# Kernel optimization log

Hardware: AMD Instinct MI355X
Metric: run time of the kernel (lower is better)

The kernel has to match this reference:

```python
import math
import jax, jax.numpy as jnp
import numpy as np

D_MODEL = 1024
HEADS = 16
B, S = 4, 2048


def setup_inputs() -> dict:
    key = jax.random.key(0)
    ks = jax.random.split(key, 8)
    scale = 1.0 / math.sqrt(D_MODEL)
    return {
        "q": jax.random.normal(ks[0], (B, S, D_MODEL), dtype=jnp.float32),
        "k": jax.random.normal(ks[1], (B, S, D_MODEL), dtype=jnp.float32),
        "v": jax.random.normal(ks[2], (B, S, D_MODEL), dtype=jnp.float32),
        "mask": jax.random.randint(ks[3], (B, S), 0, 2).astype(jnp.bool_),
        "alibi_mask": jax.random.normal(ks[4], (1, HEADS, S, S), dtype=jnp.float32),
        "Wq": jax.random.normal(ks[5], (D_MODEL, D_MODEL), dtype=jnp.float32) * scale,
        "Wk": jax.random.normal(ks[6], (D_MODEL, D_MODEL), dtype=jnp.float32) * scale,
        "Wv": jax.random.normal(ks[7], (D_MODEL, D_MODEL), dtype=jnp.float32) * scale,
    }


def _split_heads(x):
    b, s, d = x.shape
    return x.reshape(b, s, HEADS, d // HEADS).transpose(0, 2, 1, 3)  # [B,H,S,hd]


def reference(q, k, v, mask, alibi_mask, Wq, Wk, Wv):
    # QKV projections (Linear, no bias)
    qh = _split_heads(q @ Wq)
    kh = _split_heads(k @ Wk)
    vh = _split_heads(v @ Wv)
    depth = qh.shape[-1]
    # naive full attention matrix [B,H,Sq,Sk]
    w = jnp.einsum("bhqd,bhkd->bhqk", qh, kh) / math.sqrt(depth)
    # mask: [B,Sk] -> [B,1,1,Sk], True = masked
    w = jnp.where(mask[:, None, None, :], -jnp.inf, w)
    w = w + alibi_mask
    a = jax.nn.softmax(w, axis=-1)  # dropout p=0 -> identity
    out = jnp.einsum("bhqk,bhkd->bhqd", a, vh)
    # combine heads -> [B,S,D]
    out = out.transpose(0, 2, 1, 3).reshape(q.shape[0], q.shape[1], -1)
    return (out, a)
```

## Files before the change

kernel.cpp:

```cpp
#include <hip/hip_runtime.h>
#include <hip/hip_bf16.h>
#include <math.h>

constexpr int B  = 4;
constexpr int S  = 2048;
constexpr int D  = 1024;
constexpr int H  = 16;
constexpr int HD = 64;
constexpr float LOG2E  = 1.4426950408889634f;
constexpr float SCALE2 = 0.125f * LOG2E;

using f32x4 = __attribute__((ext_vector_type(4))) float;
using s16x8 = __attribute__((ext_vector_type(8))) short;
using u16x8 = __attribute__((ext_vector_type(8))) unsigned short;
using u16x4 = __attribute__((ext_vector_type(4))) unsigned short;

__device__ __forceinline__ unsigned short f2bf(float f) {
    union { float f; unsigned u; } x; x.f = f;
    unsigned r = x.u + 0x7fffu + ((x.u >> 16) & 1u);
    return (unsigned short)(r >> 16);
}
__device__ __forceinline__ unsigned short f2bf_fast(float f) {
    union { float f; unsigned u; } x; x.f = f;
    return (unsigned short)((x.u + 0x8000u) >> 16);
}
__device__ __forceinline__ float bf2f(unsigned short h) {
    union { unsigned u; float f; } x; x.u = ((unsigned)h) << 16;
    return x.f;
}
__device__ __forceinline__ float fexp2(float x) {
#if __has_builtin(__builtin_amdgcn_exp2f)
    return __builtin_amdgcn_exp2f(x);
#else
    return __expf(x * 0.6931471805599453f);
#endif
}

#define MFMA_BF16(Af, Bf, Cf) __builtin_amdgcn_mfma_f32_16x16x32_bf16(Af, Bf, Cf, 0, 0, 0)

__global__ __launch_bounds__(256) void k_wt(const float* __restrict__ W,
                                            unsigned short* __restrict__ Wt) {
    __shared__ unsigned short T[64][68];
    const int k0 = blockIdx.x * 64, n0 = blockIdx.y * 64;
    const int t = threadIdx.x;
    {
        const int kr = t >> 4, nc4 = (t & 15) * 4;
        for (int rr = 0; rr < 4; ++rr) {
            const int kk = kr + rr * 16;
            f32x4 wv = *reinterpret_cast<const f32x4*>(&W[(size_t)(k0 + kk) * D + n0 + nc4]);
#pragma unroll
            for (int j = 0; j < 4; ++j) T[nc4 + j][kk] = f2bf(wv[j]);
        }
    }
    __syncthreads();
    {
        const int nr = t >> 4, kc4 = (t & 15) * 4;
        for (int rr = 0; rr < 4; ++rr) {
            const int nn = nr + rr * 16;
            u16x4 o;
#pragma unroll
            for (int j = 0; j < 4; ++j) o[j] = T[nn][kc4 + j];
            *reinterpret_cast<u16x4*>(&Wt[(size_t)(n0 + nn) * D + k0 + kc4]) = o;
        }
    }
}

__global__ __launch_bounds__(256) void k_proj_mfma(const float* __restrict__ X,
                                                   const unsigned short* __restrict__ Wt,
                                                   unsigned short* __restrict__ Y) {
    __shared__ alignas(16) unsigned short As[128][72];
    __shared__ alignas(16) unsigned short Bs[128][72];
    const int bm = blockIdx.y * 128, bn = blockIdx.x * 128;
    const int t = threadIdx.x, w = t >> 6, l = t & 63;
    const int wr = w >> 1, wc = w & 1;
    const int lr = l & 15, lg = l >> 4;
    f32x4 acc[4][4] = {};

    for (int k0 = 0; k0 < D; k0 += 64) {
        {
            const int c4 = (t & 15) * 4;
            int row = t >> 4;
            for (int rr = 0; rr < 8; ++rr, row += 16) {
                f32x4 xv = *reinterpret_cast<const f32x4*>(&X[(size_t)(bm + row) * D + k0 + c4]);
                u16x4 hv;
#pragma unroll
                for (int j = 0; j < 4; ++j) hv[j] = f2bf(xv[j]);
                *reinterpret_cast<u16x4*>(&As[row][c4]) = hv;
            }
        }
        for (int i = 0; i < 4; ++i) {
            const int idx = t + i * 256;
            const int row = idx >> 3, c8 = (idx & 7) * 8;
            *reinterpret_cast<u16x8*>(&Bs[row][c8]) =
                *reinterpret_cast<const u16x8*>(&Wt[(size_t)(bn + row) * D + k0 + c8]);
        }
        __syncthreads();
#pragma unroll
        for (int kk = 0; kk < 2; ++kk) {
            s16x8 af[4], bf[4];
#pragma unroll
            for (int f = 0; f < 4; ++f) {
                af[f] = *reinterpret_cast<const s16x8*>(&As[wr * 64 + f * 16 + lr][kk * 32 + lg * 8]);
                bf[f] = *reinterpret_cast<const s16x8*>(&Bs[wc * 64 + f * 16 + lr][kk * 32 + lg * 8]);
            }
#pragma unroll
            for (int fm = 0; fm < 4; ++fm)
#pragma unroll
                for (int fn = 0; fn < 4; ++fn)
                    acc[fm][fn] = MFMA_BF16(af[fm], bf[fn], acc[fm][fn]);
        }
        __syncthreads();
    }
#pragma unroll
    for (int fm = 0; fm < 4; ++fm)
#pragma unroll
        for (int fn = 0; fn < 4; ++fn)
#pragma unroll
            for (int r = 0; r < 4; ++r) {
                const int m = bm + wr * 64 + fm * 16 + lg * 4 + r;
                const int n = bn + wc * 64 + fn * 16 + lr;
                const int b = m >> 11, s = m & (S - 1);
                const int h = n >> 6, e = n & 63;
                Y[(((size_t)(b * H + h) * S) + s) * HD + e] = f2bf(acc[fm][fn][r]);
            }
}

__global__ __launch_bounds__(256) void k_projv_mfma(const float* __restrict__ X,
                                                    const unsigned short* __restrict__ Wt,
                                                    unsigned short* __restrict__ VT) {
    __shared__ alignas(16) unsigned short SM[2][128][72];
    unsigned short (*As)[72] = SM[0];
    unsigned short (*Bs)[72] = SM[1];
    const int bm = blockIdx.y * 128, bn = blockIdx.x * 128;
    const int t = threadIdx.x, w = t >> 6, l = t & 63;
    const int wr = w >> 1, wc = w & 1;
    const int lr = l & 15, lg = l >> 4;
    f32x4 acc[4][4] = {};

    for (int k0 = 0; k0 < D; k0 += 64) {
        {
            const int c4 = (t & 15) * 4;
            int row = t >> 4;
            for (int rr = 0; rr < 8; ++rr, row += 16) {
                f32x4 xv = *reinterpret_cast<const f32x4*>(&X[(size_t)(bm + row) * D + k0 + c4]);
                u16x4 hv;
#pragma unroll
                for (int j = 0; j < 4; ++j) hv[j] = f2bf(xv[j]);
                *reinterpret_cast<u16x4*>(&As[row][c4]) = hv;
            }
        }
        for (int i = 0; i < 4; ++i) {
            const int idx = t + i * 256;
            const int row = idx >> 3, c8 = (idx & 7) * 8;
            *reinterpret_cast<u16x8*>(&Bs[row][c8]) =
                *reinterpret_cast<const u16x8*>(&Wt[(size_t)(bn + row) * D + k0 + c8]);
        }
        __syncthreads();
#pragma unroll
        for (int kk = 0; kk < 2; ++kk) {
            s16x8 af[4], bf[4];
#pragma unroll
            for (int f = 0; f < 4; ++f) {
                af[f] = *reinterpret_cast<const s16x8*>(&As[wr * 64 + f * 16 + lr][kk * 32 + lg * 8]);
                bf[f] = *reinterpret_cast<const s16x8*>(&Bs[wc * 64 + f * 16 + lr][kk * 32 + lg * 8]);
            }
#pragma unroll
            for (int fm = 0; fm < 4; ++fm)
#pragma unroll
                for (int fn = 0; fn < 4; ++fn)
                    acc[fm][fn] = MFMA_BF16(af[fm], bf[fn], acc[fm][fn]);
        }
        __syncthreads();
    }
    unsigned short (*T)[144] = reinterpret_cast<unsigned short(*)[144]>(&SM[0][0][0]);
#pragma unroll
    for (int fm = 0; fm < 4; ++fm)
#pragma unroll
        for (int fn = 0; fn < 4; ++fn)
#pragma unroll
            for (int r = 0; r < 4; ++r)
                T[wc * 64 + fn * 16 + lr][wr * 64 + fm * 16 + lg * 4 + r] = f2bf(acc[fm][fn][r]);
    __syncthreads();
    const int b = bm >> 11, s0 = bm & (S - 1);
    for (int it = 0; it < 8; ++it) {
        const int idx = t + it * 256;
        const int row = idx >> 4, c8 = (idx & 15) * 8;
        const int h = (bn + row) >> 6, e = (bn + row) & 63;
        *reinterpret_cast<u16x8*>(&VT[((size_t)(b * H + h) * HD + e) * S + s0 + c8]) =
            *reinterpret_cast<const u16x8*>(&T[row][c8]);
    }
}

__global__ __launch_bounds__(256) void k_abf16(const float* __restrict__ A,
                                               unsigned short* __restrict__ O) {
    const size_t N = (size_t)H * S * S;
    const size_t stride = (size_t)gridDim.x * 256 * 8;
    for (size_t i = ((size_t)blockIdx.x * 256 + threadIdx.x) * 8; i < N; i += stride) {
        f32x4 a0 = *reinterpret_cast<const f32x4*>(&A[i]);
        f32x4 a1 = *reinterpret_cast<const f32x4*>(&A[i + 4]);
        u16x8 o;
#pragma unroll
        for (int j = 0; j < 4; ++j) {
            o[j]     = f2bf(a0[j] * LOG2E);
            o[4 + j] = f2bf(a1[j] * LOG2E);
        }
        *reinterpret_cast<u16x8*>(&O[i]) = o;
    }
}

template <bool ABF16>
__global__ __launch_bounds__(512, 4) void k_sumexp(
    const unsigned short* __restrict__ QH, const unsigned short* __restrict__ KH,
    const float* __restrict__ ALIBI, const unsigned short* __restrict__ ABF,
    const int* __restrict__ MASK, float* __restrict__ INVL) {
    __shared__ alignas(16) unsigned short Ks[64][72];
    __shared__ alignas(16) unsigned short ALs[128][72];

    const int bh = blockIdx.y, b = bh >> 4, h = bh & 15;
    const int q0 = blockIdx.x * 128;
    const int t = threadIdx.x, w = t >> 6, ln = t & 63;
    const int lr = ln & 15, lg = ln >> 4;
    const unsigned short NEGBIG = f2bf(-1e30f);
    const size_t hoff = (size_t)h * S * S;

    const unsigned short* Kb = KH + (size_t)bh * S * HD;

    s16x8 qf[2];
#pragma unroll
    for (int kk = 0; kk < 2; ++kk)
        qf[kk] = *reinterpret_cast<const s16x8*>(
            &QH[((size_t)bh * S + q0 + w * 16 + lr) * HD + kk * 32 + lg * 8]);

    float psum = 0.f;

    for (int k0 = 0; k0 < S; k0 += 64) {
        {
            const int row = t >> 3, c8 = (t & 7) * 8;
            *reinterpret_cast<u16x8*>(&Ks[row][c8]) =
                *reinterpret_cast<const u16x8*>(&Kb[(size_t)(k0 + row) * HD + c8]);
        }
#pragma unroll
        for (int i = 0; i < 2; ++i) {
            const int idx = t + i * 512, row = idx >> 3, c8 = (idx & 7) * 8;
            int4 m0 = *reinterpret_cast<const int4*>(&MASK[b * S + k0 + c8]);
            int4 m1 = *reinterpret_cast<const int4*>(&MASK[b * S + k0 + c8 + 4]);
            u16x8 av;
            if constexpr (ABF16) {
                av = *reinterpret_cast<const u16x8*>(&ABF[hoff + (size_t)(q0 + row) * S + k0 + c8]);
            } else {
                f32x4 a0 = *reinterpret_cast<const f32x4*>(&ALIBI[hoff + (size_t)(q0 + row) * S + k0 + c8]);
                f32x4 a1 = *reinterpret_cast<const f32x4*>(&ALIBI[hoff + (size_t)(q0 + row) * S + k0 + c8 + 4]);
#pragma unroll
                for (int j = 0; j < 4; ++j) {
                    av[j] = f2bf(a0[j] * LOG2E);
                    av[4 + j] = f2bf(a1[j] * LOG2E);
                }
            }
            u16x8 sv;
            sv[0] = m0.x ? NEGBIG : av[0];
            sv[1] = m0.y ? NEGBIG : av[1];
            sv[2] = m0.z ? NEGBIG : av[2];
            sv[3] = m0.w ? NEGBIG : av[3];
            sv[4] = m1.x ? NEGBIG : av[4];
            sv[5] = m1.y ? NEGBIG : av[5];
            sv[6] = m1.z ? NEGBIG : av[6];
            sv[7] = m1.w ? NEGBIG : av[7];
            *reinterpret_cast<u16x8*>(&ALs[row][c8]) = sv;
        }
        __syncthreads();

        f32x4 acc[4] = {};
#pragma unroll
        for (int kk = 0; kk < 2; ++kk)
#pragma unroll
            for (int fn = 0; fn < 4; ++fn) {
                s16x8 kf = *reinterpret_cast<const s16x8*>(&Ks[fn * 16 + lr][kk * 32 + lg * 8]);
                acc[fn] = MFMA_BF16(kf, qf[kk], acc[fn]);
            }
#pragma unroll
        for (int fn = 0; fn < 4; ++fn) {
            u16x4 alv = *reinterpret_cast<const u16x4*>(&ALs[w * 16 + lr][fn * 16 + lg * 4]);
            f32x4 al;
#pragma unroll
            for (int j = 0; j < 4; ++j) al[j] = bf2f(alv[j]);
            f32x4 sv = acc[fn] * SCALE2 + al;
            psum += fexp2(sv[0]) + fexp2(sv[1]) + fexp2(sv[2]) + fexp2(sv[3]);
        }
        __syncthreads();
    }

    psum += __shfl_xor(psum, 16, 64);
    psum += __shfl_xor(psum, 32, 64);
    if (lg == 0)
        INVL[(size_t)bh * S + q0 + w * 16 + lr] = 1.0f / psum;
}

template <bool ABF16>
__global__ __launch_bounds__(512, 4) void k_attn(
    const unsigned short* __restrict__ QH, const unsigned short* __restrict__ KH,
    const unsigned short* __restrict__ VT, const float* __restrict__ ALIBI,
    const unsigned short* __restrict__ ABF, const int* __restrict__ MASK,
    const float* __restrict__ INVL, float* __restrict__ Aout,
    float* __restrict__ OUT) {
    __shared__ alignas(16) unsigned short Ks[64][72];
    __shared__ alignas(16) unsigned short Vs[64][72];
    __shared__ alignas(16) unsigned short ALs[128][72];
    __shared__ alignas(16) unsigned short Ps[128][72];

    const int bh = blockIdx.y, b = bh >> 4, h = bh & 15;
    const int q0 = blockIdx.x * 128;
    const int t = threadIdx.x, w = t >> 6, ln = t & 63;
    const int lr = ln & 15, lg = ln >> 4;
    const unsigned short NEGBIG = f2bf(-1e30f);
    const size_t hoff = (size_t)h * S * S;

    const unsigned short* Kb = KH + (size_t)bh * S * HD;
    const unsigned short* Vb = VT + (size_t)bh * HD * S;

    s16x8 qf[2];
#pragma unroll
    for (int kk = 0; kk < 2; ++kk)
        qf[kk] = *reinterpret_cast<const s16x8*>(
            &QH[((size_t)bh * S + q0 + w * 16 + lr) * HD + kk * 32 + lg * 8]);

    const float invl = INVL[(size_t)bh * S + q0 + w * 16 + lr];
    float* arow = Aout + ((size_t)bh * S + q0 + w * 16 + lr) * S;

    f32x4 oacc[4] = {};

    for (int k0 = 0; k0 < S; k0 += 64) {
        {
            const int row = t >> 3, c8 = (t & 7) * 8;
            *reinterpret_cast<u16x8*>(&Ks[row][c8]) =
                *reinterpret_cast<const u16x8*>(&Kb[(size_t)(k0 + row) * HD + c8]);
            *reinterpret_cast<u16x8*>(&Vs[row][c8]) =
                *reinterpret_cast<const u16x8*>(&Vb[(size_t)row * S + k0 + c8]);
        }
#pragma unroll
        for (int i = 0; i < 2; ++i) {
            const int idx = t + i * 512, row = idx >> 3, c8 = (idx & 7) * 8;
            int4 m0 = *reinterpret_cast<const int4*>(&MASK[b * S + k0 + c8]);
            int4 m1 = *reinterpret_cast<const int4*>(&MASK[b * S + k0 + c8 + 4]);
            u16x8 av;
            if constexpr (ABF16) {
                av = *reinterpret_cast<const u16x8*>(&ABF[hoff + (size_t)(q0 + row) * S + k0 + c8]);
            } else {
                f32x4 a0 = *reinterpret_cast<const f32x4*>(&ALIBI[hoff + (size_t)(q0 + row) * S + k0 + c8]);
                f32x4 a1 = *reinterpret_cast<const f32x4*>(&ALIBI[hoff + (size_t)(q0 + row) * S + k0 + c8 + 4]);
#pragma unroll
                for (int j = 0; j < 4; ++j) {
                    av[j] = f2bf(a0[j] * LOG2E);
                    av[4 + j] = f2bf(a1[j] * LOG2E);
                }
            }
            u16x8 sv;
            sv[0] = m0.x ? NEGBIG : av[0];
            sv[1] = m0.y ? NEGBIG : av[1];
            sv[2] = m0.z ? NEGBIG : av[2];
            sv[3] = m0.w ? NEGBIG : av[3];
            sv[4] = m1.x ? NEGBIG : av[4];
            sv[5] = m1.y ? NEGBIG : av[5];
            sv[6] = m1.z ? NEGBIG : av[6];
            sv[7] = m1.w ? NEGBIG : av[7];
            *reinterpret_cast<u16x8*>(&ALs[row][c8]) = sv;
        }
        __syncthreads();

        f32x4 acc[4] = {};
#pragma unroll
        for (int kk = 0; kk < 2; ++kk)
#pragma unroll
            for (int fn = 0; fn < 4; ++fn) {
                s16x8 kf = *reinterpret_cast<const s16x8*>(&Ks[fn * 16 + lr][kk * 32 + lg * 8]);
                acc[fn] = MFMA_BF16(kf, qf[kk], acc[fn]);
            }

#pragma unroll
        for (int fn = 0; fn < 4; ++fn) {
            u16x4 alv = *reinterpret_cast<const u16x4*>(&ALs[w * 16 + lr][fn * 16 + lg * 4]);
            f32x4 al;
#pragma unroll
            for (int j = 0; j < 4; ++j) al[j] = bf2f(alv[j]);
            f32x4 sv = acc[fn] * SCALE2 + al;
            f32x4 p;
#pragma unroll
            for (int j = 0; j < 4; ++j) p[j] = fexp2(sv[j]);
            p *= invl;
            __builtin_nontemporal_store(
                p, reinterpret_cast<f32x4*>(arow + k0 + fn * 16 + lg * 4));
            u16x4 pb;
#pragma unroll
            for (int j = 0; j < 4; ++j) pb[j] = f2bf_fast(p[j]);
            *reinterpret_cast<u16x4*>(&Ps[w * 16 + lr][fn * 16 + lg * 4]) = pb;
        }

#pragma unroll
        for (int c = 0; c < 2; ++c) {
            s16x8 pa = *reinterpret_cast<const s16x8*>(&Ps[w * 16 + lr][c * 32 + lg * 8]);
#pragma unroll
            for (int fn = 0; fn < 4; ++fn) {
                s16x8 vf = *reinterpret_cast<const s16x8*>(&Vs[fn * 16 + lr][c * 32 + lg * 8]);
                oacc[fn] = MFMA_BF16(pa, vf, oacc[fn]);
            }
        }
        __syncthreads();
    }

#pragma unroll
    for (int fn = 0; fn < 4; ++fn)
#pragma unroll
        for (int r = 0; r < 4; ++r)
            OUT[(size_t)(b * S + q0 + w * 16 + lg * 4 + r) * D + h * HD + fn * 16 + lr] =
                oacc[fn][r];
}

extern "C" void kernel_launch(void* const* d_in, const int* in_sizes, int n_in,
                              void* d_out, int out_size, void* d_ws, size_t ws_size,
                              hipStream_t stream) {
    const float* q     = (const float*)d_in[0];
    const float* k     = (const float*)d_in[1];
    const float* v     = (const float*)d_in[2];
    const int*   mask  = (const int*)d_in[3];
    const float* alibi = (const float*)d_in[4];
    const float* Wq    = (const float*)d_in[5];
    const float* Wk    = (const float*)d_in[6];
    const float* Wv    = (const float*)d_in[7];

    float* out = (float*)d_out;
    float* a   = out + (size_t)B * S * D;

    const size_t NH = (size_t)B * H * S * HD;
    unsigned short* qh  = (unsigned short*)d_ws;
    unsigned short* kh  = qh + NH;
    unsigned short* vT  = kh + NH;
    unsigned short* wqt = vT + NH;
    unsigned short* wkt = wqt + (size_t)D * D;
    unsigned short* wvt = wkt + (size_t)D * D;
    float*          invl = (float*)(wvt + (size_t)D * D);
    unsigned short* abf  = (unsigned short*)(invl + (size_t)B * H * S);

    const size_t need_bf16 =
        ((size_t)(abf - qh) + (size_t)H * S * S) * sizeof(unsigned short);
    const bool use_abf16 = ws_size >= need_bf16;

    const dim3 blk(256);

    k_wt<<<dim3(D / 64, D / 64), blk, 0, stream>>>(Wq, wqt);
    k_wt<<<dim3(D / 64, D / 64), blk, 0, stream>>>(Wk, wkt);
    k_wt<<<dim3(D / 64, D / 64), blk, 0, stream>>>(Wv, wvt);

    if (use_abf16)
        k_abf16<<<dim3(8192), blk, 0, stream>>>(alibi, abf);

    k_proj_mfma<<<dim3(D / 128, (B * S) / 128), blk, 0, stream>>>(q, wqt, qh);
    k_proj_mfma<<<dim3(D / 128, (B * S) / 128), blk, 0, stream>>>(k, wkt, kh);
    k_projv_mfma<<<dim3(D / 128, (B * S) / 128), blk, 0, stream>>>(v, wvt, vT);

    if (use_abf16) {
        k_sumexp<true><<<dim3(S / 128, B * H), dim3(512), 0, stream>>>(
            qh, kh, alibi, abf, mask, invl);
        k_attn<true><<<dim3(S / 128, B * H), dim3(512), 0, stream>>>(
            qh, kh, vT, alibi, abf, mask, invl, a, out);
    } else {
        k_sumexp<false><<<dim3(S / 128, B * H), dim3(512), 0, stream>>>(
            qh, kh, alibi, abf, mask, invl);
        k_attn<false><<<dim3(S / 128, B * H), dim3(512), 0, stream>>>(
            qh, kh, vT, alibi, abf, mask, invl, a, out);
    }
}
```

Measured before the change: 700.7 us.

## Merge projection launches, remap attention blocks across XCDs, reuse alibi LDS for P

```diff
diff --git a/kernel.cpp b/kernel.cpp
--- a/kernel.cpp
+++ b/kernel.cpp
@@ -38,8 +38,14 @@
 
 #define MFMA_BF16(Af, Bf, Cf) __builtin_amdgcn_mfma_f32_16x16x32_bf16(Af, Bf, Cf, 0, 0, 0)
 
-__global__ __launch_bounds__(256) void k_wt(const float* __restrict__ W,
-                                            unsigned short* __restrict__ Wt) {
+__global__ __launch_bounds__(256) void k_wt3(const float* __restrict__ Wq,
+                                             const float* __restrict__ Wk,
+                                             const float* __restrict__ Wv,
+                                             unsigned short* __restrict__ wqt,
+                                             unsigned short* __restrict__ wkt,
+                                             unsigned short* __restrict__ wvt) {
+    const float* W = blockIdx.z == 0 ? Wq : (blockIdx.z == 1 ? Wk : Wv);
+    unsigned short* Wt = blockIdx.z == 0 ? wqt : (blockIdx.z == 1 ? wkt : wvt);
     __shared__ unsigned short T[64][68];
     const int k0 = blockIdx.x * 64, n0 = blockIdx.y * 64;
     const int t = threadIdx.x;
@@ -65,9 +71,16 @@
     }
 }
 
-__global__ __launch_bounds__(256) void k_proj_mfma(const float* __restrict__ X,
-                                                   const unsigned short* __restrict__ Wt,
-                                                   unsigned short* __restrict__ Y) {
+__global__ __launch_bounds__(256) void k_proj2(const float* __restrict__ Xq,
+                                               const float* __restrict__ Xk,
+                                               const unsigned short* __restrict__ wqt,
+                                               const unsigned short* __restrict__ wkt,
+                                               unsigned short* __restrict__ qh,
+                                               unsigned short* __restrict__ kh) {
+    const float* X = blockIdx.z == 0 ? Xq : Xk;
+    const unsigned short* Wt = blockIdx.z == 0 ? wqt : wkt;
+    unsigned short* Y = blockIdx.z == 0 ? qh : kh;
+
     __shared__ alignas(16) unsigned short As[128][72];
     __shared__ alignas(16) unsigned short Bs[128][72];
     const int bm = blockIdx.y * 128, bn = blockIdx.x * 128;
@@ -216,8 +229,10 @@
     __shared__ alignas(16) unsigned short Ks[64][72];
     __shared__ alignas(16) unsigned short ALs[128][72];
 
-    const int bh = blockIdx.y, b = bh >> 4, h = bh & 15;
-    const int q0 = blockIdx.x * 128;
+    const int bid = blockIdx.x;
+    const int wg = (bid & 7) * 128 + (bid >> 3);
+    const int bh = wg >> 4, b = bh >> 4, h = bh & 15;
+    const int q0 = (wg & 15) * 128;
     const int t = threadIdx.x, w = t >> 6, ln = t & 63;
     const int lr = ln & 15, lg = ln >> 4;
     const unsigned short NEGBIG = f2bf(-1e30f);
@@ -305,10 +320,11 @@
     __shared__ alignas(16) unsigned short Ks[64][72];
     __shared__ alignas(16) unsigned short Vs[64][72];
     __shared__ alignas(16) unsigned short ALs[128][72];
-    __shared__ alignas(16) unsigned short Ps[128][72];
-
-    const int bh = blockIdx.y, b = bh >> 4, h = bh & 15;
-    const int q0 = blockIdx.x * 128;
+
+    const int bid = blockIdx.x;
+    const int wg = (bid & 7) * 128 + (bid >> 3);
+    const int bh = wg >> 4, b = bh >> 4, h = bh & 15;
+    const int q0 = (wg & 15) * 128;
     const int t = threadIdx.x, w = t >> 6, ln = t & 63;
     const int lr = ln & 15, lg = ln >> 4;
     const unsigned short NEGBIG = f2bf(-1e30f);
@@ -391,12 +407,12 @@
             u16x4 pb;
 #pragma unroll
             for (int j = 0; j < 4; ++j) pb[j] = f2bf_fast(p[j]);
-            *reinterpret_cast<u16x4*>(&Ps[w * 16 + lr][fn * 16 + lg * 4]) = pb;
+            *reinterpret_cast<u16x4*>(&ALs[w * 16 + lr][fn * 16 + lg * 4]) = pb;
         }
 
 #pragma unroll
         for (int c = 0; c < 2; ++c) {
-            s16x8 pa = *reinterpret_cast<const s16x8*>(&Ps[w * 16 + lr][c * 32 + lg * 8]);
+            s16x8 pa = *reinterpret_cast<const s16x8*>(&ALs[w * 16 + lr][c * 32 + lg * 8]);
 #pragma unroll
             for (int fn = 0; fn < 4; ++fn) {
                 s16x8 vf = *reinterpret_cast<const s16x8*>(&Vs[fn * 16 + lr][c * 32 + lg * 8]);
@@ -445,26 +461,23 @@
 
     const dim3 blk(256);
 
-    k_wt<<<dim3(D / 64, D / 64), blk, 0, stream>>>(Wq, wqt);
-    k_wt<<<dim3(D / 64, D / 64), blk, 0, stream>>>(Wk, wkt);
-    k_wt<<<dim3(D / 64, D / 64), blk, 0, stream>>>(Wv, wvt);
+    k_wt3<<<dim3(D / 64, D / 64, 3), blk, 0, stream>>>(Wq, Wk, Wv, wqt, wkt, wvt);
 
     if (use_abf16)
         k_abf16<<<dim3(8192), blk, 0, stream>>>(alibi, abf);
 
-    k_proj_mfma<<<dim3(D / 128, (B * S) / 128), blk, 0, stream>>>(q, wqt, qh);
-    k_proj_mfma<<<dim3(D / 128, (B * S) / 128), blk, 0, stream>>>(k, wkt, kh);
+    k_proj2<<<dim3(D / 128, (B * S) / 128, 2), blk, 0, stream>>>(q, k, wqt, wkt, qh, kh);
     k_projv_mfma<<<dim3(D / 128, (B * S) / 128), blk, 0, stream>>>(v, wvt, vT);
 
     if (use_abf16) {
-        k_sumexp<true><<<dim3(S / 128, B * H), dim3(512), 0, stream>>>(
+        k_sumexp<true><<<dim3(1024), dim3(512), 0, stream>>>(
             qh, kh, alibi, abf, mask, invl);
-        k_attn<true><<<dim3(S / 128, B * H), dim3(512), 0, stream>>>(
+        k_attn<true><<<dim3(1024), dim3(512), 0, stream>>>(
             qh, kh, vT, alibi, abf, mask, invl, a, out);
     } else {
-        k_sumexp<false><<<dim3(S / 128, B * H), dim3(512), 0, stream>>>(
+        k_sumexp<false><<<dim3(1024), dim3(512), 0, stream>>>(
             qh, kh, alibi, abf, mask, invl);
-        k_attn<false><<<dim3(S / 128, B * H), dim3(512), 0, stream>>>(
+        k_attn<false><<<dim3(1024), dim3(512), 0, stream>>>(
             qh, kh, vT, alibi, abf, mask, invl, a, out);
     }
 }
```

New measurement: 665.3 us. -5.0%, faster.
